# Kernel optimization log

Measured on AMD Instinct MI355X. Metric: run time of the kernel, lower is better.

Reference implementation:

```python
import jax, jax.numpy as jnp
import numpy as np

RES = (64, 64)
TEMP = 0.1  # forward default temp

def _mgrid(res):
    # matches torch.meshgrid(linspace(0, r-1, r)...) with default 'ij' indexing
    gs = jnp.meshgrid(*[jnp.arange(r, dtype=jnp.float32) for r in res], indexing='ij')
    return jnp.stack(gs, 0)  # [2, H, W]

def setup_inputs() -> dict:
    key = jax.random.key(0)
    k1, k2 = jax.random.split(key)
    x = jax.random.normal(k1, (8, 32, RES[0], RES[1]), dtype=jnp.float32)
    of = jax.random.normal(k2, (8, 2, RES[0], RES[1]), dtype=jnp.float32)
    return {"x": x, "of": of}

def reference(x, of):
    bs, C = x.shape[0], x.shape[1]
    hw = RES[0] * RES[1]
    gpos = _mgrid(RES).reshape(2, hw)                 # [2, HW] target pixel positions
    opos = gpos[None] + of.reshape(bs, 2, hw)         # [bs, 2, HW] flow-displaced source positions
    # L1 distance: logits[b, i, j] = sum_c |opos[b, c, j] - gpos[c, i]|
    dist = jnp.abs(opos[:, :, None, :] - gpos[None, :, :, None]).sum(axis=1)  # [bs, HW, HW]
    # softmax over target axis i (dim=-2 in torch) -> each source pixel j distributes mass over targets
    locs = jax.nn.softmax(-dist / TEMP, axis=1)       # [bs, HW, HW]
    # out[b, c, i] = sum_j x[b, c, j] * locs[b, i, j]
    out = jnp.einsum('bij,bcj->bci', locs, x.reshape(bs, C, hw))
    return out.reshape(bs, C, RES[0], RES[1])
```

## Files before the change

### kernel.cpp

```cpp
#include <hip/hip_runtime.h>
#include <hip/hip_fp16.h>
#include <math.h>

#define HW    4096
#define NC    32
#define NB    8
#define TINV  10.0f
#define RWIN  8
#define WDIM  (8 + 2 * RWIN)
#define RCUT  2.0f


__device__ __forceinline__ __half2 u32_as_h2(unsigned int u) {
    union { unsigned int u; __half2 h; } c; c.u = u; return c.h;
}
__device__ __forceinline__ unsigned int h2_as_u32(__half2 h) {
    union { __half2 h; unsigned int u; } c; c.h = h; return c.u;
}

__global__ __launch_bounds__(256) void prep_kernel(
    const float* __restrict__ x, const float* __restrict__ of,
    float4* __restrict__ params, __half2* __restrict__ xt2)
{
    __shared__ float tile[16][66];
    const int bx   = blockIdx.x;
    const int half = blockIdx.y;
    const int b    = bx >> 6;
    const int j0   = (bx & 63) << 6;
    const int t    = threadIdx.x;
    const int ch0  = half << 4;
    const int jj   = t & 63;
    const int c4   = t >> 6;

    if (half == 0 && t < 64) {
        int j = j0 + t;
        float oy = (float)(j >> 6) + of[(b * 2 + 0) * HW + j];
        float ox = (float)(j & 63) + of[(b * 2 + 1) * HW + j];
        int cy0 = min(max((int)floorf(oy), 0), 63);
        int cx0 = min(max((int)floorf(ox), 0), 63);
        float Dy = 0.f, Dx = 0.f;
        #pragma unroll
        for (int d = -3; d <= 3; ++d) {
            int iy = cy0 + d, ix = cx0 + d;
            if ((unsigned)iy < 64u) Dy += __expf(-TINV * fabsf(oy - (float)iy));
            if ((unsigned)ix < 64u) Dx += __expf(-TINV * fabsf(ox - (float)ix));
        }
        params[(b << 12) + j] = make_float4(oy, ox, 1.f / Dy, 1.f / Dx);
    }

    #pragma unroll
    for (int k = 0; k < 4; ++k) {
        int c = c4 * 4 + k;
        tile[c][jj] = x[((size_t)(b * NC + ch0 + c) << 12) + j0 + jj];
    }
    __syncthreads();
    #pragma unroll
    for (int k = 0; k < 2; ++k) {
        int s  = k * 256 + t;
        int j2 = s >> 3, pr = s & 7;
        xt2[((size_t)((b << 12) + j0 + j2) << 4) + (half << 3) + pr] =
            __floats2half2_rn(tile[2 * pr][j2], tile[2 * pr + 1][j2]);
    }
}

__global__ __launch_bounds__(256) void gather_kernel(
    const float4* __restrict__ params, const unsigned int* __restrict__ xtu,
    float* __restrict__ out)
{
    __shared__ float4       wp[4][65];
    __shared__ int          sj[4][64];
    __shared__ unsigned int pool[4 * 64 * 17];

    const int b    = blockIdx.y;
    const int tile = blockIdx.x;
    const int ty0  = (tile >> 3) << 3;
    const int tx0  = (tile & 7) << 3;

    const int tid  = threadIdx.x;
    const int lane = tid & 63;
    const int wv   = __builtin_amdgcn_readfirstlane(tid >> 6);

    const float iy = (float)(ty0 + (lane >> 3));
    const float ix = (float)(tx0 + (lane & 7));

    __half2 acc16[16];
    #pragma unroll
    for (int c = 0; c < 16; ++c) acc16[c] = __floats2half2_rn(0.f, 0.f);

    const float4*       pb = params + (b << 12);
    const unsigned int* xb = xtu + ((size_t)(b << 12) << 4);

    const int srow = lane >> 5;
    const int scol = lane & 31;

    unsigned int* XSu = pool;

    for (int r = 0; r < 3; ++r) {
        int ry = wv + srow * 4 + r * 8;
        int jy = ty0 - RWIN + ry;
        int jx = tx0 - RWIN + scol;
        bool valid = ((unsigned)jy < 64u) && ((unsigned)jx < 64u) && (scol < WDIM);
        int j = (jy << 6) + jx;
        float4 p = pb[valid ? j : 0];
        float cy = fminf(fmaxf(p.x, 0.f), 63.f);
        float cx = fminf(fmaxf(p.y, 0.f), 63.f);
        float dyr = fmaxf(fmaxf((float)ty0 - cy, cy - ((float)ty0 + 7.f)), 0.f);
        float dxr = fmaxf(fmaxf((float)tx0 - cx, cx - ((float)tx0 + 7.f)), 0.f);
        bool pred = valid && (dyr + dxr < RCUT);

        unsigned long long m = __ballot(pred);
        int cnt = __popcll(m);
        if (pred) {
            int pos = __builtin_amdgcn_mbcnt_hi((unsigned)(m >> 32),
                      __builtin_amdgcn_mbcnt_lo((unsigned)m, 0u));
            wp[wv][pos] = p;
            sj[wv][pos] = j;
        }
        if (lane == cnt) wp[wv][cnt] = make_float4(1.f, 1.f, 0.f, 0.f);
        int cntp = cnt + (cnt & 1);

        for (int m4 = 0; m4 < cntp; m4 += 16) {
            int s = m4 + (lane >> 2);
            if (s < cntp) {
                int jj = sj[wv][min(s, cnt - 1)];
                const uint4* src = (const uint4*)(xb + (size_t)jj * 16 + ((lane & 3) << 2));
                *(uint4*)&XSu[(((wv << 6) + s) << 4) + ((lane & 3) << 2)] = *src;
            }
        }

        for (int k = 0; k < cntp; k += 2) {
            float4 p0 = wp[wv][k], p1 = wp[wv][k + 1];
            const uint4* x0 = (const uint4*)&XSu[((wv << 6) + k)     << 4];
            const uint4* x1 = (const uint4*)&XSu[((wv << 6) + k + 1) << 4];
            uint4 A[4], B[4];
            #pragma unroll
            for (int q = 0; q < 4; ++q) { A[q] = x0[q]; B[q] = x1[q]; }

            float g0 = (__expf(-TINV * fabsf(p0.x - iy)) * p0.z)
                     * (__expf(-TINV * fabsf(p0.y - ix)) * p0.w);
            float g1 = (__expf(-TINV * fabsf(p1.x - iy)) * p1.z)
                     * (__expf(-TINV * fabsf(p1.y - ix)) * p1.w);
            __half2 hg0 = __float2half2_rn(g0);
            __half2 hg1 = __float2half2_rn(g1);

            #pragma unroll
            for (int q = 0; q < 4; ++q) {
                acc16[4 * q + 0] = __hfma2(hg0, u32_as_h2(A[q].x), acc16[4 * q + 0]);
                acc16[4 * q + 1] = __hfma2(hg0, u32_as_h2(A[q].y), acc16[4 * q + 1]);
                acc16[4 * q + 2] = __hfma2(hg0, u32_as_h2(A[q].z), acc16[4 * q + 2]);
                acc16[4 * q + 3] = __hfma2(hg0, u32_as_h2(A[q].w), acc16[4 * q + 3]);
            }
            #pragma unroll
            for (int q = 0; q < 4; ++q) {
                acc16[4 * q + 0] = __hfma2(hg1, u32_as_h2(B[q].x), acc16[4 * q + 0]);
                acc16[4 * q + 1] = __hfma2(hg1, u32_as_h2(B[q].y), acc16[4 * q + 1]);
                acc16[4 * q + 2] = __hfma2(hg1, u32_as_h2(B[q].z), acc16[4 * q + 2]);
                acc16[4 * q + 3] = __hfma2(hg1, u32_as_h2(B[q].w), acc16[4 * q + 3]);
            }
        }
    }

    __syncthreads();
    unsigned int* redu = pool;
    unsigned int* myr  = redu + (unsigned)tid * 17;
    #pragma unroll
    for (int c = 0; c < 16; ++c) myr[c] = h2_as_u32(acc16[c]);
    __syncthreads();

    int t  = tid & 63;
    int c0 = tid >> 6;
    #pragma unroll
    for (int k = 0; k < 4; ++k) {
        int c2 = c0 + (k << 2);
        float sx = 0.f, sy = 0.f;
        #pragma unroll
        for (int w = 0; w < 4; ++w) {
            float2 f = __half22float2(u32_as_h2(redu[(unsigned)((w << 6) + t) * 17 + c2]));
            sx += f.x; sy += f.y;
        }
        int ch   = c2 << 1;
        int base = (((b << 5) + ch) << 12) + (ty0 + (t >> 3)) * 64 + (tx0 + (t & 7));
        out[base]      = sx;
        out[base + HW] = sy;
    }
}

extern "C" void kernel_launch(void* const* d_in, const int* in_sizes, int n_in,
                              void* d_out, int out_size, void* d_ws, size_t ws_size,
                              hipStream_t stream) {
    const float* x  = (const float*)d_in[0];
    const float* of = (const float*)d_in[1];
    float* out = (float*)d_out;

    float4*  params = (float4*)d_ws;
    __half2* xt2    = (__half2*)((char*)d_ws + NB * HW * sizeof(float4));

    prep_kernel<<<dim3(NB * 64, 2), dim3(256), 0, stream>>>(x, of, params, xt2);
    gather_kernel<<<dim3(64, NB), dim3(256), 0, stream>>>(
        params, (const unsigned int*)xt2, out);
}
```

Baseline: 67.86 us.

## Compact candidates across rows and double-buffer gathered x rows in LDS

Each wave now compacts candidate source pixels from all three window rows into one list before computing, then processes them in chunks of 32. The global gathers for the next chunk are issued before computing the current chunk and written to a second LDS buffer afterwards. This is meant to hide global-load latency and cut the per-row serialization between gathering and FMA work. It costs more LDS (a fixed cap of 148 candidates per wave) and more registers held across the compute loop, which may lower occupancy. Any overflow past the cap would be unsafe.

```diff
diff --git a/kernel.cpp b/kernel.cpp
--- a/kernel.cpp
+++ b/kernel.cpp
@@ -9,6 +9,7 @@
 #define RWIN  8
 #define WDIM  (8 + 2 * RWIN)
 #define RCUT  2.0f
+#define MAXS  148
 
 
 __device__ __forceinline__ __half2 u32_as_h2(unsigned int u) {
@@ -67,9 +68,7 @@
     const float4* __restrict__ params, const unsigned int* __restrict__ xtu,
     float* __restrict__ out)
 {
-    __shared__ float4       wp[4][65];
-    __shared__ int          sj[4][64];
-    __shared__ unsigned int pool[4 * 64 * 17];
+    __shared__ __align__(16) unsigned int pool[4 * MAXS * 4 + 4 * MAXS + 4096];
 
     const int b    = blockIdx.y;
     const int tile = blockIdx.x;
@@ -80,6 +79,10 @@
     const int lane = tid & 63;
     const int wv   = __builtin_amdgcn_readfirstlane(tid >> 6);
 
+    float4*       wpW = ((float4*)pool) + wv * MAXS;
+    int*          sjW = ((int*)pool) + 4 * MAXS * 4 + wv * MAXS;
+    unsigned int* XSW = pool + 4 * MAXS * 4 + 4 * MAXS + wv * 1024;
+
     const float iy = (float)(ty0 + (lane >> 3));
     const float ix = (float)(tx0 + (lane & 7));
 
@@ -93,70 +96,100 @@
     const int srow = lane >> 5;
     const int scol = lane & 31;
 
-    unsigned int* XSu = pool;
-
+    float4 pr3[3]; int jr3[3]; bool va3[3];
+    #pragma unroll
     for (int r = 0; r < 3; ++r) {
         int ry = wv + srow * 4 + r * 8;
         int jy = ty0 - RWIN + ry;
         int jx = tx0 - RWIN + scol;
         bool valid = ((unsigned)jy < 64u) && ((unsigned)jx < 64u) && (scol < WDIM);
         int j = (jy << 6) + jx;
-        float4 p = pb[valid ? j : 0];
+        va3[r] = valid; jr3[r] = j;
+        pr3[r] = pb[valid ? j : 0];
+    }
+
+    int total = 0;
+    #pragma unroll
+    for (int r = 0; r < 3; ++r) {
+        float4 p = pr3[r];
         float cy = fminf(fmaxf(p.x, 0.f), 63.f);
         float cx = fminf(fmaxf(p.y, 0.f), 63.f);
         float dyr = fmaxf(fmaxf((float)ty0 - cy, cy - ((float)ty0 + 7.f)), 0.f);
         float dxr = fmaxf(fmaxf((float)tx0 - cx, cx - ((float)tx0 + 7.f)), 0.f);
-        bool pred = valid && (dyr + dxr < RCUT);
-
+        bool pred = va3[r] && (dyr + dxr < RCUT);
         unsigned long long m = __ballot(pred);
-        int cnt = __popcll(m);
         if (pred) {
-            int pos = __builtin_amdgcn_mbcnt_hi((unsigned)(m >> 32),
-                      __builtin_amdgcn_mbcnt_lo((unsigned)m, 0u));
-            wp[wv][pos] = p;
-            sj[wv][pos] = j;
-        }
-        if (lane == cnt) wp[wv][cnt] = make_float4(1.f, 1.f, 0.f, 0.f);
-        int cntp = cnt + (cnt & 1);
-
-        for (int m4 = 0; m4 < cntp; m4 += 16) {
-            int s = m4 + (lane >> 2);
-            if (s < cntp) {
-                int jj = sj[wv][min(s, cnt - 1)];
-                const uint4* src = (const uint4*)(xb + (size_t)jj * 16 + ((lane & 3) << 2));
-                *(uint4*)&XSu[(((wv << 6) + s) << 4) + ((lane & 3) << 2)] = *src;
+            int pos = total + __builtin_amdgcn_mbcnt_hi((unsigned)(m >> 32),
+                              __builtin_amdgcn_mbcnt_lo((unsigned)m, 0u));
+            wpW[pos] = p;
+            sjW[pos] = jr3[r];
+        }
+        total += __popcll(m);
+    }
+    if ((total & 1) && lane == 0) {
+        wpW[total] = make_float4(1.f, 1.f, 0.f, 0.f);
+        sjW[total] = sjW[0];
+    }
+    const int padT = total + (total & 1);
+    const int nch  = (padT + 31) >> 5;
+
+    auto stage_load = [&](int c, uint4& A, uint4& B) {
+        int s = (c << 5) + (lane >> 1);
+        A = make_uint4(0u, 0u, 0u, 0u); B = A;
+        if (s < padT) {
+            const unsigned int* src = xb + (size_t)sjW[s] * 16 + ((lane & 1) << 3);
+            A = *(const uint4*)src;
+            B = *(const uint4*)(src + 4);
+        }
+    };
+    auto stage_write = [&](int c, uint4 A, uint4 B) {
+        unsigned int* d = XSW + ((c & 1) << 9) + (lane << 3);
+        *(uint4*)d       = A;
+        *(uint4*)(d + 4) = B;
+    };
+
+    if (nch > 0) {
+        uint4 a0, b0;
+        stage_load(0, a0, b0);
+        stage_write(0, a0, b0);
+        for (int c = 0; c < nch; ++c) {
+            uint4 na, nb;
+            const bool more = (c + 1) < nch;
+            if (more) stage_load(c + 1, na, nb);
+
+            int cnt_c = min(32, padT - (c << 5));
+            const uint4* XR = (const uint4*)(XSW + ((c & 1) << 9));
+            for (int k = 0; k < cnt_c; k += 2) {
+                float4 p0 = wpW[(c << 5) + k], p1 = wpW[(c << 5) + k + 1];
+                const uint4* x0 = XR + (k << 2);
+                const uint4* x1 = XR + ((k + 1) << 2);
+                uint4 A[4], Bv[4];
+                #pragma unroll
+                for (int q = 0; q < 4; ++q) { A[q] = x0[q]; Bv[q] = x1[q]; }
+
+                float g0 = (__expf(-TINV * fabsf(p0.x - iy)) * p0.z)
+                         * (__expf(-TINV * fabsf(p0.y - ix)) * p0.w);
+                float g1 = (__expf(-TINV * fabsf(p1.x - iy)) * p1.z)
+                         * (__expf(-TINV * fabsf(p1.y - ix)) * p1.w);
+                __half2 hg0 = __float2half2_rn(g0);
+                __half2 hg1 = __float2half2_rn(g1);
+
+                #pragma unroll
+                for (int q = 0; q < 4; ++q) {
+                    acc16[4 * q + 0] = __hfma2(hg0, u32_as_h2(A[q].x), acc16[4 * q + 0]);
+                    acc16[4 * q + 1] = __hfma2(hg0, u32_as_h2(A[q].y), acc16[4 * q + 1]);
+                    acc16[4 * q + 2] = __hfma2(hg0, u32_as_h2(A[q].z), acc16[4 * q + 2]);
+                    acc16[4 * q + 3] = __hfma2(hg0, u32_as_h2(A[q].w), acc16[4 * q + 3]);
+                }
+                #pragma unroll
+                for (int q = 0; q < 4; ++q) {
+                    acc16[4 * q + 0] = __hfma2(hg1, u32_as_h2(Bv[q].x), acc16[4 * q + 0]);
+                    acc16[4 * q + 1] = __hfma2(hg1, u32_as_h2(Bv[q].y), acc16[4 * q + 1]);
+                    acc16[4 * q + 2] = __hfma2(hg1, u32_as_h2(Bv[q].z), acc16[4 * q + 2]);
+                    acc16[4 * q + 3] = __hfma2(hg1, u32_as_h2(Bv[q].w), acc16[4 * q + 3]);
+                }
             }
-        }
-
-        for (int k = 0; k < cntp; k += 2) {
-            float4 p0 = wp[wv][k], p1 = wp[wv][k + 1];
-            const uint4* x0 = (const uint4*)&XSu[((wv << 6) + k)     << 4];
-            const uint4* x1 = (const uint4*)&XSu[((wv << 6) + k + 1) << 4];
-            uint4 A[4], B[4];
-            #pragma unroll
-            for (int q = 0; q < 4; ++q) { A[q] = x0[q]; B[q] = x1[q]; }
-
-            float g0 = (__expf(-TINV * fabsf(p0.x - iy)) * p0.z)
-                     * (__expf(-TINV * fabsf(p0.y - ix)) * p0.w);
-            float g1 = (__expf(-TINV * fabsf(p1.x - iy)) * p1.z)
-                     * (__expf(-TINV * fabsf(p1.y - ix)) * p1.w);
-            __half2 hg0 = __float2half2_rn(g0);
-            __half2 hg1 = __float2half2_rn(g1);
-
-            #pragma unroll
-            for (int q = 0; q < 4; ++q) {
-                acc16[4 * q + 0] = __hfma2(hg0, u32_as_h2(A[q].x), acc16[4 * q + 0]);
-                acc16[4 * q + 1] = __hfma2(hg0, u32_as_h2(A[q].y), acc16[4 * q + 1]);
-                acc16[4 * q + 2] = __hfma2(hg0, u32_as_h2(A[q].z), acc16[4 * q + 2]);
-                acc16[4 * q + 3] = __hfma2(hg0, u32_as_h2(A[q].w), acc16[4 * q + 3]);
-            }
-            #pragma unroll
-            for (int q = 0; q < 4; ++q) {
-                acc16[4 * q + 0] = __hfma2(hg1, u32_as_h2(B[q].x), acc16[4 * q + 0]);
-                acc16[4 * q + 1] = __hfma2(hg1, u32_as_h2(B[q].y), acc16[4 * q + 1]);
-                acc16[4 * q + 2] = __hfma2(hg1, u32_as_h2(B[q].z), acc16[4 * q + 2]);
-                acc16[4 * q + 3] = __hfma2(hg1, u32_as_h2(B[q].w), acc16[4 * q + 3]);
-            }
+            if (more) stage_write(c + 1, na, nb);
         }
     }
 
```

After: 66.57 us. No clear change (-1.9%).
